# Kernel optimization log

Measured on AMD Instinct MI355X. Metric: run time of the kernel, lower is better.

Reference implementation:

```python
import jax, jax.numpy as jnp
import numpy as np

V, B, L, NG = 50000, 128, 350, 3        # vocab, batch(docs), doc length, n-gram window
D, H, C = 768, 256, 20                  # bert dim, num_hidden, class_num
HEADS, LAYERS, K, ALPHA = 8, 2, 3, 0.15 # GAT heads/layers, diffusion hops k, alpha


def setup_inputs() -> dict:
    rng = np.random.default_rng(0)
    # per-doc graphs: 350 unique word-ids per doc (nodes), n-gram window edges
    node_ids = np.stack([rng.choice(V, L, replace=False) for _ in range(B)]).ravel()
    src_b, dst_b = [], []
    for i in range(L):
        for j in range(max(0, i - NG), min(L, i + NG + 1)):
            src_b.append(i); dst_b.append(j)
    src_b, dst_b = np.asarray(src_b), np.asarray(dst_b)
    off = (np.arange(B) * L)[:, None]
    edge_src = (src_b[None, :] + off).ravel()
    edge_dst = (dst_b[None, :] + off).ravel()
    graph_id = np.repeat(np.arange(B), L)

    ks = jax.random.split(jax.random.key(0), 8)
    f32 = jnp.float32
    return {
        'node_ids': jnp.asarray(node_ids, jnp.int32),
        'edge_src': jnp.asarray(edge_src, jnp.int32),
        'edge_dst': jnp.asarray(edge_dst, jnp.int32),
        'graph_id': jnp.asarray(graph_id, jnp.int32),
        'emb':    (jax.random.normal(ks[0], (V, D), f32) * 0.02),
        'W1':     (jax.random.normal(ks[1], (D, H), f32) / np.sqrt(D)).astype(f32),
        'b1':     jnp.zeros((H,), f32),
        'W2':     (jax.random.normal(ks[2], (H, C), f32) / np.sqrt(H)).astype(f32),
        'b2':     jnp.zeros((C,), f32),
        'gat_W':  (jax.random.normal(ks[3], (LAYERS, HEADS, C, C), f32) / np.sqrt(C)).astype(f32),
        'a_src':  (jax.random.normal(ks[4], (LAYERS, HEADS, C), f32) * 0.1),
        'a_dst':  (jax.random.normal(ks[5], (LAYERS, HEADS, C), f32) * 0.1),
        'w_gate': (jax.random.normal(ks[6], (C,), f32) / np.sqrt(C)).astype(f32),
        'b_gate': jnp.zeros((), f32),
    }


def _gat_layer(h, W, a_s, a_d, src, dst, N):
    # h: [N,C]; W: [Hd,C,C]; a_s/a_d: [Hd,C]
    z = jnp.einsum('nc,hcd->hnd', h, W)                     # [Hd,N,C]
    e = jax.nn.leaky_relu(jnp.einsum('hnd,hd->hn', z, a_s)[:, src]
                          + jnp.einsum('hnd,hd->hn', z, a_d)[:, dst], 0.2)  # [Hd,E]

    def segsoftmax(ev):  # edge softmax over incoming edges at each dst node
        m = jax.ops.segment_max(ev, dst, num_segments=N)
        ex = jnp.exp(ev - m[dst])
        s = jax.ops.segment_sum(ex, dst, num_segments=N)
        return ex / (s[dst] + 1e-9)

    att = jax.vmap(segsoftmax)(e)                           # [Hd,E]

    def diffuse(zh, ah):  # attention diffusion: Z_t = (1-a) A Z_{t-1} + a Z_0
        zt = zh
        for _ in range(K):
            agg = jax.ops.segment_sum(ah[:, None] * zt[src], dst, num_segments=N)
            zt = (1.0 - ALPHA) * agg + ALPHA * zh
        return zt

    out = jax.vmap(diffuse)(z, att)                         # [Hd,N,C]
    return jax.nn.elu(out).mean(axis=0)                     # merge='mean'


def reference(node_ids, edge_src, edge_dst, graph_id, emb, W1, b1, W2, b2,
              gat_W, a_src, a_dst, w_gate, b_gate):
    N = node_ids.shape[0]
    x = emb[node_ids]                                       # [N,768] gather
    x = jax.nn.relu(x @ W1 + b1)                            # linear1 + ReLU
    h = x @ W2 + b2                                         # linear2 -> [N,C]
    for l in range(LAYERS):
        h = _gat_layer(h, gat_W[l], a_src[l], a_dst[l], edge_src, edge_dst, N)
    gate = jax.nn.sigmoid(h @ w_gate + b_gate)[:, None]     # WeightAndSum gate
    return jax.ops.segment_sum(gate * h, graph_id, num_segments=B)  # [B,C]
```

## Files before the change

### kernel.cpp

```cpp
#include <hip/hip_runtime.h>
#include <hip/hip_bf16.h>
#include <cstddef>

#define NB_NODES 44800
#define NDOCS 128
#define DLEN 350
#define DIM 768
#define HID 256
#define NCLS 20
#define NHEADS 8
#define ZSTR 24

typedef __bf16 v8bf __attribute__((ext_vector_type(8)));
typedef __bf16 v4bf __attribute__((ext_vector_type(4)));
typedef float v4f __attribute__((ext_vector_type(4)));

__global__ __launch_bounds__(256) void k_transpose(const float* __restrict__ W1,
                                                   __bf16* __restrict__ W1T) {
  int idx = blockIdx.x * 256 + threadIdx.x;
  int n = idx / 768, k = idx - n * 768;
  W1T[idx] = (__bf16)W1[k * 256 + n];
}

__global__ __launch_bounds__(256) void k_mlp(
    const int* __restrict__ node_ids, const float* __restrict__ emb,
    const __bf16* __restrict__ W1T, const float* __restrict__ b1,
    const float* __restrict__ W2, const float* __restrict__ b2,
    float* __restrict__ h0) {
  __shared__ __align__(16) char smem[43520];
  __bf16* As = (__bf16*)smem;
  float*  xs = (float*)smem;
  __bf16* w2s = (__bf16*)(smem + 33280);
  int tid = threadIdx.x;
  int wave = tid >> 6, lane = tid & 63;
  int quad = lane >> 4, l16 = lane & 15;
  int m0 = blockIdx.x * 64;

  int lrow = tid & 15;
  int lk4  = (tid >> 4) & 3;
  int khalf = (tid >> 6) & 1;
  int msubA = tid >> 7;
  int kbase = khalf * 32 + lk4 * 8;
  const float* apA = emb + (size_t)node_ids[m0 + msubA * 16 + lrow] * DIM + kbase;
  const float* apB = emb + (size_t)node_ids[m0 + (msubA + 2) * 16 + lrow] * DIM + kbase;

  v4f acc[4][4];
#pragma unroll
  for (int ms = 0; ms < 4; ++ms)
#pragma unroll
    for (int j = 0; j < 4; ++j) acc[ms][j] = (v4f){0.f, 0.f, 0.f, 0.f};

  v4f pf[4];
  pf[0] = *(const v4f*)(apA); pf[1] = *(const v4f*)(apA + 4);
  pf[2] = *(const v4f*)(apB); pf[3] = *(const v4f*)(apB + 4);

  for (int kc = 0; kc < 12; ++kc) {
    __bf16* buf = As + (kc & 1) * 4096;
    v8bf w0, w1;
#pragma unroll
    for (int e = 0; e < 4; ++e) {
      w0[e] = (__bf16)pf[0][e]; w0[4 + e] = (__bf16)pf[1][e];
      w1[e] = (__bf16)pf[2][e]; w1[4 + e] = (__bf16)pf[3][e];
    }
    *(v8bf*)(buf + tid * 8) = w0;
    *(v8bf*)(buf + tid * 8 + 2048) = w1;
    if (kc < 11) {
      int k1 = (kc + 1) * 64;
      pf[0] = *(const v4f*)(apA + k1); pf[1] = *(const v4f*)(apA + k1 + 4);
      pf[2] = *(const v4f*)(apB + k1); pf[3] = *(const v4f*)(apB + k1 + 4);
    }
    __syncthreads();

#pragma unroll
    for (int ks = 0; ks < 2; ++ks) {
      v8bf af[4], bv[4];
#pragma unroll
      for (int ms = 0; ms < 4; ++ms)
        af[ms] = *(const v8bf*)(buf + ((ms * 2 + ks) * 64 + lane) * 8);
#pragma unroll
      for (int j = 0; j < 4; ++j)
        bv[j] = *(const v8bf*)(W1T + (size_t)(wave * 64 + j * 16 + l16) * DIM + kc * 64 + ks * 32 + quad * 8);
#pragma unroll
      for (int ms = 0; ms < 4; ++ms)
#pragma unroll
        for (int j = 0; j < 4; ++j)
          acc[ms][j] = __builtin_amdgcn_mfma_f32_16x16x32_bf16(af[ms], bv[j], acc[ms][j], 0, 0, 0);
    }
  }

  __syncthreads();
  for (int i = tid; i < HID * NCLS; i += 256) w2s[i] = (__bf16)W2[i];

#pragma unroll
  for (int p = 0; p < 2; ++p) {
    if (p) __syncthreads();
#pragma unroll
    for (int mh = 0; mh < 2; ++mh) {
      int ms = p * 2 + mh;
#pragma unroll
      for (int j = 0; j < 4; ++j) {
        int col = wave * 64 + j * 16 + l16;
        float bb = b1[col];
#pragma unroll
        for (int r = 0; r < 4; ++r) {
          int lr = mh * 16 + quad * 4 + r;
          float v = acc[ms][j][r] + bb;
          xs[lr * 260 + col] = v > 0.f ? v : 0.f;
        }
      }
    }
    __syncthreads();
    if (tid < 160) {
      int m = tid / 5, c0 = (tid % 5) * 4;
      v4f s = *(const v4f*)(b2 + c0);
      for (int k = 0; k < HID; ++k) {
        float x = xs[m * 260 + k];
        v4bf w = *(const v4bf*)(w2s + k * NCLS + c0);
        s[0] += x * (float)w[0]; s[1] += x * (float)w[1];
        s[2] += x * (float)w[2]; s[3] += x * (float)w[3];
      }
      *(v4f*)(h0 + (size_t)(m0 + p * 32 + m) * NCLS + c0) = s;
    }
  }
}

__global__ __launch_bounds__(384) void k_gat(
    const float* __restrict__ hin, const float* __restrict__ gatW,
    const float* __restrict__ a_src, const float* __restrict__ a_dst,
    int layer, float* __restrict__ zout) {
  __shared__ float zA[DLEN * ZSTR];
  __shared__ float asv[DLEN], adv[DLEN];
  int tid = threadIdx.x;
  int head = blockIdx.x & 7;
  int doc = blockIdx.x >> 3;
  const float* W  = gatW  + (size_t)(layer * NHEADS + head) * NCLS * NCLS;
  const float* av = a_src + (layer * NHEADS + head) * NCLS;
  const float* dv = a_dst + (layer * NHEADS + head) * NCLS;
  int r = tid;
  bool act = r < DLEN;

  float z0[NCLS];
  if (act) {
    const float* hr = hin + ((size_t)doc * DLEN + r) * NCLS;
    float h[NCLS];
#pragma unroll
    for (int q = 0; q < 5; ++q) {
      v4f t = *(const v4f*)(hr + q * 4);
#pragma unroll
      for (int e = 0; e < 4; ++e) h[q * 4 + e] = t[e];
    }
    float zacc[NCLS];
#pragma unroll
    for (int d = 0; d < NCLS; ++d) zacc[d] = 0.f;
#pragma unroll
    for (int c = 0; c < NCLS; ++c) {
      float hc = h[c];
#pragma unroll
      for (int d = 0; d < NCLS; ++d) zacc[d] += hc * W[c * NCLS + d];
    }
    float sa = 0.f, sd = 0.f;
#pragma unroll
    for (int d = 0; d < NCLS; ++d) { sa += zacc[d] * av[d]; sd += zacc[d] * dv[d]; }
    asv[r] = sa; adv[r] = sd;
#pragma unroll
    for (int q = 0; q < 5; ++q) {
      v4f t;
#pragma unroll
      for (int e = 0; e < 4; ++e) t[e] = zacc[q * 4 + e];
      *(v4f*)(zA + r * ZSTR + q * 4) = t;
    }
#pragma unroll
    for (int d = 0; d < NCLS; ++d) z0[d] = zacc[d];
  }
  __syncthreads();

  float att[7];
  if (act) {
    float ad = adv[r];
    float e[7]; float m = -1e30f;
#pragma unroll
    for (int j = 0; j < 7; ++j) {
      int s = r - 3 + j;
      bool valid = (s >= 0) && (s < DLEN);
      float x = valid ? asv[s] + ad : -1e30f;
      x = x > 0.f ? x : 0.2f * x;
      e[j] = valid ? x : -1e30f;
      if (e[j] > m) m = e[j];
    }
    float sum = 0.f;
#pragma unroll
    for (int j = 0; j < 7; ++j) {
      float ex = (e[j] > -1e29f) ? expf(e[j] - m) : 0.f;
      e[j] = ex; sum += ex;
    }
    float inv = 1.f / (sum + 1e-9f);
#pragma unroll
    for (int j = 0; j < 7; ++j) att[j] = e[j] * inv;
  }

  float vn[NCLS];
  for (int hop = 0; hop < 3; ++hop) {
    if (act) {
      v4f agg[5];
#pragma unroll
      for (int q = 0; q < 5; ++q) agg[q] = (v4f){0.f, 0.f, 0.f, 0.f};
#pragma unroll
      for (int j = 0; j < 7; ++j) {
        int s = r - 3 + j;
        s = s < 0 ? 0 : (s > DLEN - 1 ? DLEN - 1 : s);
        float a = att[j];
#pragma unroll
        for (int q = 0; q < 5; ++q) {
          v4f zq = *(const v4f*)(zA + s * ZSTR + q * 4);
#pragma unroll
          for (int e = 0; e < 4; ++e) agg[q][e] += a * zq[e];
        }
      }
#pragma unroll
      for (int q = 0; q < 5; ++q)
#pragma unroll
        for (int e = 0; e < 4; ++e)
          vn[q * 4 + e] = 0.85f * agg[q][e] + 0.15f * z0[q * 4 + e];
    }
    if (hop < 2) {
      __syncthreads();
      if (act) {
#pragma unroll
        for (int q = 0; q < 5; ++q) {
          v4f t;
#pragma unroll
          for (int e = 0; e < 4; ++e) t[e] = vn[q * 4 + e];
          *(v4f*)(zA + r * ZSTR + q * 4) = t;
        }
      }
      __syncthreads();
    }
  }

  if (act) {
    float* og = zout + ((size_t)head * NB_NODES + (size_t)doc * DLEN + r) * NCLS;
#pragma unroll
    for (int q = 0; q < 5; ++q) {
      v4f t;
#pragma unroll
      for (int e = 0; e < 4; ++e) {
        float x = vn[q * 4 + e];
        t[e] = x > 0.f ? x : expf(x) - 1.f;
      }
      *(v4f*)(og + q * 4) = t;
    }
  }
}

__global__ __launch_bounds__(256) void k_headmean(
    const float* __restrict__ eluzt, float* __restrict__ hout) {
  int idx = blockIdx.x * 256 + threadIdx.x;
  v4f s = (v4f){0.f, 0.f, 0.f, 0.f};
#pragma unroll
  for (int h = 0; h < NHEADS; ++h)
    s += ((const v4f*)eluzt)[(size_t)h * (NB_NODES * NCLS / 4) + idx];
  v4f o; o[0] = s[0] * 0.125f; o[1] = s[1] * 0.125f; o[2] = s[2] * 0.125f; o[3] = s[3] * 0.125f;
  ((v4f*)hout)[idx] = o;
}

__global__ __launch_bounds__(64) void k_pool(
    const float* __restrict__ hfin, const float* __restrict__ w_gate,
    const float* __restrict__ b_gate, float* __restrict__ out) {
  int b = blockIdx.x, lane = threadIdx.x;
  float wg[NCLS];
#pragma unroll
  for (int c = 0; c < NCLS; ++c) wg[c] = w_gate[c];
  float bg = b_gate[0];
  float acc[NCLS];
#pragma unroll
  for (int c = 0; c < NCLS; ++c) acc[c] = 0.f;
  for (int n = lane; n < DLEN; n += 64) {
    const v4f* hr = (const v4f*)(hfin + ((size_t)b * DLEN + n) * NCLS);
    float hv[NCLS];
    float d = bg;
#pragma unroll
    for (int q = 0; q < 5; ++q) {
      v4f t = hr[q];
#pragma unroll
      for (int j = 0; j < 4; ++j) { hv[q * 4 + j] = t[j]; d += t[j] * wg[q * 4 + j]; }
    }
    float g = 1.f / (1.f + expf(-d));
#pragma unroll
    for (int c = 0; c < NCLS; ++c) acc[c] += g * hv[c];
  }
#pragma unroll
  for (int off = 32; off > 0; off >>= 1)
#pragma unroll
    for (int c = 0; c < NCLS; ++c) acc[c] += __shfl_down(acc[c], off);
  if (lane == 0)
#pragma unroll
    for (int c = 0; c < NCLS; ++c) out[b * NCLS + c] = acc[c];
}

extern "C" void kernel_launch(void* const* d_in, const int* in_sizes, int n_in,
                              void* d_out, int out_size, void* d_ws, size_t ws_size,
                              hipStream_t stream) {
  const int* node_ids = (const int*)d_in[0];
  const float* emb    = (const float*)d_in[4];
  const float* W1     = (const float*)d_in[5];
  const float* b1     = (const float*)d_in[6];
  const float* W2     = (const float*)d_in[7];
  const float* b2     = (const float*)d_in[8];
  const float* gatW   = (const float*)d_in[9];
  const float* a_src  = (const float*)d_in[10];
  const float* a_dst  = (const float*)d_in[11];
  const float* w_gate = (const float*)d_in[12];
  const float* b_gate = (const float*)d_in[13];
  float* out = (float*)d_out;
  char* ws = (char*)d_ws;

  __bf16* W1T = (__bf16*)(ws + 0);
  float* hA  = (float*)(ws + 393216);
  float* hB  = (float*)(ws + 3977216);
  float* zt  = (float*)(ws + 7561216);

  k_transpose<<<768, 256, 0, stream>>>(W1, W1T);
  k_mlp<<<NB_NODES / 64, 256, 0, stream>>>(node_ids, emb, W1T, b1, W2, b2, hA);
  k_gat<<<NDOCS * NHEADS, 384, 0, stream>>>(hA, gatW, a_src, a_dst, 0, zt);
  k_headmean<<<(NB_NODES * NCLS / 4) / 256, 256, 0, stream>>>(zt, hB);
  k_gat<<<NDOCS * NHEADS, 384, 0, stream>>>(hB, gatW, a_src, a_dst, 1, zt);
  k_headmean<<<(NB_NODES * NCLS / 4) / 256, 256, 0, stream>>>(zt, hA);
  k_pool<<<NDOCS, 64, 0, stream>>>(hA, w_gate, b_gate, out);
}
```

Measured before the change: 361.3 us.

## Fuse both GAT layers, head mean and pooling into one per-document kernel

Replaces the per-(doc,head) GAT kernels, head-mean kernels and pooling kernel with a single kernel where each block handles one document. It loops over layers and heads, accumulating the ELU head mean in registers, then computes the gated sum pooling with a block reduction. This removes intermediate global writes and reads and several launches. In exchange the grid shrinks to 128 blocks and the heads are processed serially, which reduces parallelism across the GPU.

After: 462.3 us. +27.9%, slower.

```diff
diff --git a/kernel.cpp b/kernel.cpp
--- a/kernel.cpp
+++ b/kernel.cpp
@@ -124,177 +124,175 @@
   }
 }
 
-__global__ __launch_bounds__(384) void k_gat(
+__global__ __launch_bounds__(384) void k_gat_all(
     const float* __restrict__ hin, const float* __restrict__ gatW,
     const float* __restrict__ a_src, const float* __restrict__ a_dst,
-    int layer, float* __restrict__ zout) {
+    const float* __restrict__ w_gate, const float* __restrict__ b_gate,
+    float* __restrict__ out) {
   __shared__ float zA[DLEN * ZSTR];
   __shared__ float asv[DLEN], adv[DLEN];
+  __shared__ float red[6][NCLS];
   int tid = threadIdx.x;
-  int head = blockIdx.x & 7;
-  int doc = blockIdx.x >> 3;
-  const float* W  = gatW  + (size_t)(layer * NHEADS + head) * NCLS * NCLS;
-  const float* av = a_src + (layer * NHEADS + head) * NCLS;
-  const float* dv = a_dst + (layer * NHEADS + head) * NCLS;
+  int doc = blockIdx.x;
   int r = tid;
   bool act = r < DLEN;
 
-  float z0[NCLS];
+  float h[NCLS];
   if (act) {
     const float* hr = hin + ((size_t)doc * DLEN + r) * NCLS;
-    float h[NCLS];
 #pragma unroll
     for (int q = 0; q < 5; ++q) {
       v4f t = *(const v4f*)(hr + q * 4);
 #pragma unroll
       for (int e = 0; e < 4; ++e) h[q * 4 + e] = t[e];
     }
-    float zacc[NCLS];
-#pragma unroll
-    for (int d = 0; d < NCLS; ++d) zacc[d] = 0.f;
-#pragma unroll
-    for (int c = 0; c < NCLS; ++c) {
-      float hc = h[c];
-#pragma unroll
-      for (int d = 0; d < NCLS; ++d) zacc[d] += hc * W[c * NCLS + d];
-    }
-    float sa = 0.f, sd = 0.f;
-#pragma unroll
-    for (int d = 0; d < NCLS; ++d) { sa += zacc[d] * av[d]; sd += zacc[d] * dv[d]; }
-    asv[r] = sa; adv[r] = sd;
-#pragma unroll
-    for (int q = 0; q < 5; ++q) {
-      v4f t;
-#pragma unroll
-      for (int e = 0; e < 4; ++e) t[e] = zacc[q * 4 + e];
-      *(v4f*)(zA + r * ZSTR + q * 4) = t;
-    }
-#pragma unroll
-    for (int d = 0; d < NCLS; ++d) z0[d] = zacc[d];
-  }
-  __syncthreads();
-
-  float att[7];
-  if (act) {
-    float ad = adv[r];
-    float e[7]; float m = -1e30f;
-#pragma unroll
-    for (int j = 0; j < 7; ++j) {
-      int s = r - 3 + j;
-      bool valid = (s >= 0) && (s < DLEN);
-      float x = valid ? asv[s] + ad : -1e30f;
-      x = x > 0.f ? x : 0.2f * x;
-      e[j] = valid ? x : -1e30f;
-      if (e[j] > m) m = e[j];
-    }
-    float sum = 0.f;
-#pragma unroll
-    for (int j = 0; j < 7; ++j) {
-      float ex = (e[j] > -1e29f) ? expf(e[j] - m) : 0.f;
-      e[j] = ex; sum += ex;
-    }
-    float inv = 1.f / (sum + 1e-9f);
-#pragma unroll
-    for (int j = 0; j < 7; ++j) att[j] = e[j] * inv;
-  }
-
-  float vn[NCLS];
-  for (int hop = 0; hop < 3; ++hop) {
-    if (act) {
-      v4f agg[5];
-#pragma unroll
-      for (int q = 0; q < 5; ++q) agg[q] = (v4f){0.f, 0.f, 0.f, 0.f};
-#pragma unroll
-      for (int j = 0; j < 7; ++j) {
-        int s = r - 3 + j;
-        s = s < 0 ? 0 : (s > DLEN - 1 ? DLEN - 1 : s);
-        float a = att[j];
-#pragma unroll
-        for (int q = 0; q < 5; ++q) {
-          v4f zq = *(const v4f*)(zA + s * ZSTR + q * 4);
-#pragma unroll
-          for (int e = 0; e < 4; ++e) agg[q][e] += a * zq[e];
-        }
-      }
-#pragma unroll
-      for (int q = 0; q < 5; ++q)
-#pragma unroll
-        for (int e = 0; e < 4; ++e)
-          vn[q * 4 + e] = 0.85f * agg[q][e] + 0.15f * z0[q * 4 + e];
-    }
-    if (hop < 2) {
-      __syncthreads();
+  }
+
+#pragma unroll 1
+  for (int l = 0; l < 2; ++l) {
+    float accm[NCLS];
+#pragma unroll
+    for (int c = 0; c < NCLS; ++c) accm[c] = 0.f;
+
+#pragma unroll 1
+    for (int hd = 0; hd < NHEADS; ++hd) {
+      const float* W  = gatW  + (size_t)(l * NHEADS + hd) * NCLS * NCLS;
+      const float* av = a_src + (l * NHEADS + hd) * NCLS;
+      const float* dv = a_dst + (l * NHEADS + hd) * NCLS;
+
+      float z0[NCLS];
       if (act) {
+        float zacc[NCLS];
+#pragma unroll
+        for (int d = 0; d < NCLS; ++d) zacc[d] = 0.f;
+#pragma unroll
+        for (int c = 0; c < NCLS; ++c) {
+          float hc = h[c];
+#pragma unroll
+          for (int d = 0; d < NCLS; ++d) zacc[d] += hc * W[c * NCLS + d];
+        }
+        float sa = 0.f, sd = 0.f;
+#pragma unroll
+        for (int d = 0; d < NCLS; ++d) { sa += zacc[d] * av[d]; sd += zacc[d] * dv[d]; }
+        asv[r] = sa; adv[r] = sd;
 #pragma unroll
         for (int q = 0; q < 5; ++q) {
           v4f t;
 #pragma unroll
-          for (int e = 0; e < 4; ++e) t[e] = vn[q * 4 + e];
+          for (int e = 0; e < 4; ++e) t[e] = zacc[q * 4 + e];
           *(v4f*)(zA + r * ZSTR + q * 4) = t;
         }
+#pragma unroll
+        for (int d = 0; d < NCLS; ++d) z0[d] = zacc[d];
       }
       __syncthreads();
-    }
-  }
-
+
+      float att[7];
+      if (act) {
+        float ad = adv[r];
+        float e[7]; float m = -1e30f;
+#pragma unroll
+        for (int j = 0; j < 7; ++j) {
+          int s = r - 3 + j;
+          bool valid = (s >= 0) && (s < DLEN);
+          float x = valid ? asv[s] + ad : -1e30f;
+          x = x > 0.f ? x : 0.2f * x;
+          e[j] = valid ? x : -1e30f;
+          if (e[j] > m) m = e[j];
+        }
+        float sum = 0.f;
+#pragma unroll
+        for (int j = 0; j < 7; ++j) {
+          float ex = (e[j] > -1e29f) ? expf(e[j] - m) : 0.f;
+          e[j] = ex; sum += ex;
+        }
+        float inv = 1.f / (sum + 1e-9f);
+#pragma unroll
+        for (int j = 0; j < 7; ++j) att[j] = e[j] * inv;
+      }
+
+      float vn[NCLS];
+      for (int hop = 0; hop < 3; ++hop) {
+        if (act) {
+          v4f agg[5];
+#pragma unroll
+          for (int q = 0; q < 5; ++q) agg[q] = (v4f){0.f, 0.f, 0.f, 0.f};
+#pragma unroll
+          for (int j = 0; j < 7; ++j) {
+            int s = r - 3 + j;
+            s = s < 0 ? 0 : (s > DLEN - 1 ? DLEN - 1 : s);
+            float a = att[j];
+#pragma unroll
+            for (int q = 0; q < 5; ++q) {
+              v4f zq = *(const v4f*)(zA + s * ZSTR + q * 4);
+#pragma unroll
+              for (int e = 0; e < 4; ++e) agg[q][e] += a * zq[e];
+            }
+          }
+#pragma unroll
+          for (int q = 0; q < 5; ++q)
+#pragma unroll
+            for (int e = 0; e < 4; ++e)
+              vn[q * 4 + e] = 0.85f * agg[q][e] + 0.15f * z0[q * 4 + e];
+        }
+        if (hop < 2) {
+          __syncthreads();
+          if (act) {
+#pragma unroll
+            for (int q = 0; q < 5; ++q) {
+              v4f t;
+#pragma unroll
+              for (int e = 0; e < 4; ++e) t[e] = vn[q * 4 + e];
+              *(v4f*)(zA + r * ZSTR + q * 4) = t;
+            }
+          }
+          __syncthreads();
+        }
+      }
+
+      if (act) {
+#pragma unroll
+        for (int c = 0; c < NCLS; ++c) {
+          float x = vn[c];
+          accm[c] += x > 0.f ? x : expf(x) - 1.f;
+        }
+      }
+      __syncthreads();
+    }
+
+#pragma unroll
+    for (int c = 0; c < NCLS; ++c) h[c] = accm[c] * 0.125f;
+  }
+
+  float wg[NCLS];
+#pragma unroll
+  for (int c = 0; c < NCLS; ++c) wg[c] = w_gate[c];
+  float contrib[NCLS];
+#pragma unroll
+  for (int c = 0; c < NCLS; ++c) contrib[c] = 0.f;
   if (act) {
-    float* og = zout + ((size_t)head * NB_NODES + (size_t)doc * DLEN + r) * NCLS;
-#pragma unroll
-    for (int q = 0; q < 5; ++q) {
-      v4f t;
-#pragma unroll
-      for (int e = 0; e < 4; ++e) {
-        float x = vn[q * 4 + e];
-        t[e] = x > 0.f ? x : expf(x) - 1.f;
-      }
-      *(v4f*)(og + q * 4) = t;
-    }
-  }
-}
-
-__global__ __launch_bounds__(256) void k_headmean(
-    const float* __restrict__ eluzt, float* __restrict__ hout) {
-  int idx = blockIdx.x * 256 + threadIdx.x;
-  v4f s = (v4f){0.f, 0.f, 0.f, 0.f};
-#pragma unroll
-  for (int h = 0; h < NHEADS; ++h)
-    s += ((const v4f*)eluzt)[(size_t)h * (NB_NODES * NCLS / 4) + idx];
-  v4f o; o[0] = s[0] * 0.125f; o[1] = s[1] * 0.125f; o[2] = s[2] * 0.125f; o[3] = s[3] * 0.125f;
-  ((v4f*)hout)[idx] = o;
-}
-
-__global__ __launch_bounds__(64) void k_pool(
-    const float* __restrict__ hfin, const float* __restrict__ w_gate,
-    const float* __restrict__ b_gate, float* __restrict__ out) {
-  int b = blockIdx.x, lane = threadIdx.x;
-  float wg[NCLS];
-#pragma unroll
-  for (int c = 0; c < NCLS; ++c) wg[c] = w_gate[c];
-  float bg = b_gate[0];
-  float acc[NCLS];
-#pragma unroll
-  for (int c = 0; c < NCLS; ++c) acc[c] = 0.f;
-  for (int n = lane; n < DLEN; n += 64) {
-    const v4f* hr = (const v4f*)(hfin + ((size_t)b * DLEN + n) * NCLS);
-    float hv[NCLS];
-    float d = bg;
-#pragma unroll
-    for (int q = 0; q < 5; ++q) {
-      v4f t = hr[q];
-#pragma unroll
-      for (int j = 0; j < 4; ++j) { hv[q * 4 + j] = t[j]; d += t[j] * wg[q * 4 + j]; }
-    }
+    float d = b_gate[0];
+#pragma unroll
+    for (int c = 0; c < NCLS; ++c) d += h[c] * wg[c];
     float g = 1.f / (1.f + expf(-d));
 #pragma unroll
-    for (int c = 0; c < NCLS; ++c) acc[c] += g * hv[c];
+    for (int c = 0; c < NCLS; ++c) contrib[c] = g * h[c];
   }
 #pragma unroll
   for (int off = 32; off > 0; off >>= 1)
 #pragma unroll
-    for (int c = 0; c < NCLS; ++c) acc[c] += __shfl_down(acc[c], off);
+    for (int c = 0; c < NCLS; ++c) contrib[c] += __shfl_down(contrib[c], off);
+  int wave = tid >> 6, lane = tid & 63;
   if (lane == 0)
 #pragma unroll
-    for (int c = 0; c < NCLS; ++c) out[b * NCLS + c] = acc[c];
+    for (int c = 0; c < NCLS; ++c) red[wave][c] = contrib[c];
+  __syncthreads();
+  if (tid < NCLS) {
+    float s = 0.f;
+#pragma unroll
+    for (int w = 0; w < 6; ++w) s += red[w][tid];
+    out[doc * NCLS + tid] = s;
+  }
 }
 
 extern "C" void kernel_launch(void* const* d_in, const int* in_sizes, int n_in,
@@ -316,14 +314,8 @@
 
   __bf16* W1T = (__bf16*)(ws + 0);
   float* hA  = (float*)(ws + 393216);
-  float* hB  = (float*)(ws + 3977216);
-  float* zt  = (float*)(ws + 7561216);
 
   k_transpose<<<768, 256, 0, stream>>>(W1, W1T);
   k_mlp<<<NB_NODES / 64, 256, 0, stream>>>(node_ids, emb, W1T, b1, W2, b2, hA);
-  k_gat<<<NDOCS * NHEADS, 384, 0, stream>>>(hA, gatW, a_src, a_dst, 0, zt);
-  k_headmean<<<(NB_NODES * NCLS / 4) / 256, 256, 0, stream>>>(zt, hB);
-  k_gat<<<NDOCS * NHEADS, 384, 0, stream>>>(hB, gatW, a_src, a_dst, 1, zt);
-  k_headmean<<<(NB_NODES * NCLS / 4) / 256, 256, 0, stream>>>(zt, hA);
-  k_pool<<<NDOCS, 64, 0, stream>>>(hA, w_gate, b_gate, out);
+  k_gat_all<<<NDOCS, 384, 0, stream>>>(hA, gatW, a_src, a_dst, w_gate, b_gate, out);
 }
```
